# Kernel optimization log

Measured on AMD Instinct MI355X. Metric: run time of the kernel, lower is better.

The kernel has to match this reference:

```python
import jax, jax.numpy as jnp
import numpy as np

NEG = -1e9


def setup_inputs() -> dict:
    key = jax.random.key(0)
    ks = jax.random.split(key, 9)
    B, L, S, E = 8, 2048, 2048, 1024
    H, G, KD, VD = 16, 64, 1024, 1024
    return {
        "query": jax.random.normal(ks[0], (B, L, E), jnp.float32),
        "key": jax.random.normal(ks[1], (B, S, E), jnp.float32),
        "value": jax.random.normal(ks[2], (B, S, E), jnp.float32),
        "other": jnp.zeros((1,), jnp.float32),
        "key_padding_mask": jax.random.bernoulli(ks[3], 0.1, (B, S)),
        "nhead": H,
        "query_proj": jax.random.normal(ks[4], (1, E, KD), jnp.float32) * 0.02,
        "key_proj": jax.random.normal(ks[5], (1, E, KD), jnp.float32) * 0.02,
        "value_proj": jax.random.normal(ks[6], (1, E, VD), jnp.float32) * 0.02,
        "importance_proj": jax.random.normal(ks[7], (1, E, H * G), jnp.float32) * 0.02,
        "output_proj": jax.random.normal(ks[8], (1, VD, E), jnp.float32) * 0.02,
    }


def reference(query, key, value, other, key_padding_mask, nhead,
              query_proj, key_proj, value_proj, importance_proj, output_proj):
    B, L, E = query.shape
    S = key.shape[1]
    H = nhead
    KD = query_proj.shape[-1]
    VD = value_proj.shape[-1]
    Ek, Ev = KD // H, VD // H
    G = importance_proj.shape[-1] // H
    scale = 1.0 / jnp.sqrt(jnp.asarray(Ek, query.dtype))

    # projections -> (B, H, L/S, d)
    qs = (query @ query_proj[0]).reshape(B, L, H, Ek).transpose(0, 2, 1, 3)
    kk = (key @ key_proj[0]).reshape(B, S, H, Ek).transpose(0, 2, 1, 3)
    vs = (value @ value_proj[0]).reshape(B, S, H, Ev).transpose(0, 2, 1, 3)

    # importance-weighted global queries: softmax over L
    ips = (query @ importance_proj[0]).reshape(B, L, H, G).transpose(0, 2, 3, 1)  # (B,H,G,L)
    ips = jax.nn.softmax(ips, axis=-1)
    gqs = jnp.einsum('bhgl,bhld->bhgd', ips, qs)  # (B,H,G,Ek)

    # stage 1: global queries attend over all keys (shared attn for keys & values)
    g_scores = jnp.einsum('bhgd,bhsd->bhgs', gqs, kk) * scale  # (B,H,G,S)
    g_scores = jnp.where(key_padding_mask[:, None, None, :], NEG, g_scores)
    g_attn = jax.nn.softmax(g_scores, axis=-1)
    global_keys = jnp.einsum('bhgs,bhsd->bhgd', g_attn, kk)   # (B,H,G,Ek)
    global_values = jnp.einsum('bhgs,bhsd->bhgd', g_attn, vs)  # (B,H,G,Ev)

    # stage 2: local queries attend over G global keys/values
    l_scores = jnp.einsum('bhld,bhgd->bhlg', qs, global_keys) * scale  # (B,H,L,G)
    l_attn = jax.nn.softmax(l_scores, axis=-1)
    out = jnp.einsum('bhlg,bhgd->bhld', l_attn, global_values)  # (B,H,L,Ev)

    out = out.transpose(0, 2, 1, 3).reshape(B, L, H * Ev)
    out = out @ output_proj[0]  # (B,L,E)
    return (out, l_attn)
```

## Files before the change

kernel.cpp:

```cpp
#include <hip/hip_runtime.h>


typedef float f32x4 __attribute__((ext_vector_type(4)));
typedef _Float16 f16x8 __attribute__((ext_vector_type(8)));
typedef unsigned short u16;

#define DEV static __device__ __forceinline__

DEV u16 f2h(float x){
  _Float16 h = (_Float16)x;
  return __builtin_bit_cast(u16, h);
}
DEV float h2f(u16 u){
  return (float)__builtin_bit_cast(_Float16, u);
}
DEV void split1h(float x, u16 &h, u16 &l){
  h = f2h(x);
  l = f2h(x - h2f(h));
}
DEV unsigned pk2h(float a, float b){
  return (unsigned)f2h(a) | ((unsigned)f2h(b) << 16);
}

DEV void gload16(const u16* src, u16* dst_lds){
  __builtin_amdgcn_global_load_lds(
      (__attribute__((address_space(1))) void*)src,
      (__attribute__((address_space(3))) void*)dst_lds, 16, 0, 0);
}

__global__ __launch_bounds__(256)
void mask_norm(const unsigned char* __restrict__ src, unsigned char* __restrict__ dst, int n)
{
  const unsigned* w = (const unsigned*)src;
  const int tid = threadIdx.x;
  int local = 0;
  for (int i = tid; i < n/4; i += 256){
    unsigned v = w[i];
    if (v == 0x3F800000u) local |= 2;
    else if (v > 1u)      local |= 1;
  }
  __shared__ int red[256];
  red[tid] = local;
  __syncthreads();
  for (int s = 128; s; s >>= 1){
    if (tid < s) red[tid] |= red[tid+s];
    __syncthreads();
  }
  const int r = red[0];
  const int mode = (r & 2) ? 2 : ((r & 1) ? 1 : 0);
  for (int i = tid; i < n; i += 256){
    unsigned char v;
    if (mode == 1) v = src[i] ? 1 : 0;
    else           v = w[i]   ? 1 : 0;
    dst[i] = v;
  }
}

__global__ __launch_bounds__(256)
void conv_hi2(const float* __restrict__ x0, u16* __restrict__ h0,
              const float* __restrict__ x1, u16* __restrict__ h1, int n8)
{
  const float* x = blockIdx.z ? x1 : x0;
  u16* hi = blockIdx.z ? h1 : h0;
  const int i = blockIdx.x*256 + threadIdx.x;
  if (i >= n8) return;
  f32x4 a = ((const f32x4*)x)[2*i], b = ((const f32x4*)x)[2*i+1];
  uint4 uh;
  uh.x = pk2h(a[0], a[1]); uh.y = pk2h(a[2], a[3]);
  uh.z = pk2h(b[0], b[1]); uh.w = pk2h(b[2], b[3]);
  ((uint4*)hi)[i] = uh;
}

__global__ __launch_bounds__(256)
void conv_hi(const float* __restrict__ x, u16* __restrict__ hi, int n8)
{
  const int i = blockIdx.x*256 + threadIdx.x;
  if (i >= n8) return;
  f32x4 a = ((const f32x4*)x)[2*i], b = ((const f32x4*)x)[2*i+1];
  uint4 uh;
  uh.x = pk2h(a[0], a[1]); uh.y = pk2h(a[2], a[3]);
  uh.z = pk2h(b[0], b[1]); uh.w = pk2h(b[2], b[3]);
  ((uint4*)hi)[i] = uh;
}

__global__ __launch_bounds__(256)
void transpose_hi5(const float* __restrict__ s0, const float* __restrict__ s1,
                   const float* __restrict__ s2, const float* __restrict__ s3,
                   const float* __restrict__ s4,
                   u16* __restrict__ d0, u16* __restrict__ d1, u16* __restrict__ d2,
                   u16* __restrict__ d3, u16* __restrict__ d4)
{
  const int z = blockIdx.z;
  const float* Wsrc = z == 0 ? s0 : z == 1 ? s1 : z == 2 ? s2 : z == 3 ? s3 : s4;
  u16* Whi = z == 0 ? d0 : z == 1 ? d1 : z == 2 ? d2 : z == 3 ? d3 : d4;
  __shared__ float t[64][65];
  const int tid = threadIdx.x;
  const int n0 = blockIdx.x * 64, k0 = blockIdx.y * 64;
  #pragma unroll
  for (int it = 0; it < 16; ++it){
    int e = it*256 + tid, r = e >> 6, c = e & 63;
    t[r][c] = Wsrc[(long)(k0+r)*1024 + (n0+c)];
  }
  __syncthreads();
  #pragma unroll
  for (int it = 0; it < 16; ++it){
    int e = it*256 + tid, r = e >> 6, c = e & 63;
    Whi[(long)(n0+r)*1024 + (k0+c)] = f2h(t[c][r]);
  }
}

template<int TM, int TERMS, int CM, int EPI, int SWZ>
__global__ __launch_bounds__(256)
void gemm_g(const u16* __restrict__ Ah_g, const u16* __restrict__ Al_g,
            const u16* __restrict__ Bh_g,
            void* __restrict__ Cp, void* __restrict__ Cp2,
            const unsigned char* __restrict__ maskp,
            int K, int lda, int ldb, int ldc,
            long aB, long aH, long bB, long bH, long cB, long cH,
            int H2, int Ssz, float scale)
{
  constexpr int BN = 128, BK = 32;
  constexpr int WM = TM/2, WN = BN/2;
  constexpr int FM = WM/16, FN = WN/16;
  __shared__ __align__(16) u16 AhS[2][TM*BK];
  __shared__ __align__(16) u16 AlS[2][TERMS == 2 ? TM*BK : 8];
  __shared__ __align__(16) u16 BhS[2][BN*BK];

  const int tid = threadIdx.x;
  int bx = blockIdx.x, by = blockIdx.y;
  if constexpr (SWZ){
    const int gx = gridDim.x;
    const int nwg = gx * gridDim.y;
    const int q = nwg >> 3;
    const int flat = bx + gx * by;
    const int nf = (flat & 7) * q + (flat >> 3);
    bx = nf % gx; by = nf / gx;
  }
  const int batch = blockIdx.z;
  const int b = batch / H2, h = batch - b*H2;
  const long aOff = (long)b*aB + (long)h*aH;
  const long bOff = (long)b*bB + (long)h*bH;
  const long cOff = (long)b*cB + (long)h*cH;
  const int nBase = bx * BN;
  const int mBase = by * TM;
  const int wave = tid >> 6, lane = tid & 63;
  const int wm = wave >> 1, wn = wave & 1;
  const int cg8 = (lane & 3) * 8;
  const int rsub = lane >> 2;

  auto stage = [&](int buf, int k0){
    #pragma unroll
    for (int c = 0; c < TM/64; ++c){
      const int chunk = wave*(TM/64) + c;
      const long g = aOff + (long)(mBase + chunk*16 + rsub)*lda + k0 + cg8;
      gload16(Ah_g + g, &AhS[buf][chunk*512]);
      if constexpr (TERMS == 2) gload16(Al_g + g, &AlS[buf][chunk*512]);
    }
    #pragma unroll
    for (int c = 0; c < 2; ++c){
      const int chunk = wave*2 + c;
      const long g = bOff + (long)(nBase + chunk*16 + rsub)*ldb + k0 + cg8;
      gload16(Bh_g + g, &BhS[buf][chunk*512]);
    }
  };

  f32x4 acc[FM][FN] = {};

  stage(0, 0);
  __syncthreads();
  const int nk = K >> 5;
  for (int t = 0; t < nk; ++t){
    const int buf = t & 1;
    if (t + 1 < nk) stage(buf ^ 1, (t + 1) << 5);

    f16x8 ah[FM], al[FM], bh[FN];
    #pragma unroll
    for (int mi = 0; mi < FM; ++mi){
      const int off = (wm*WM + mi*16 + (lane & 15))*BK + (lane >> 4)*8;
      ah[mi] = *(const f16x8*)&AhS[buf][off];
      if constexpr (TERMS == 2) al[mi] = *(const f16x8*)&AlS[buf][off];
    }
    #pragma unroll
    for (int ni = 0; ni < FN; ++ni){
      const int off = (wn*WN + ni*16 + (lane & 15))*BK + (lane >> 4)*8;
      bh[ni] = *(const f16x8*)&BhS[buf][off];
    }
    #pragma unroll
    for (int mi = 0; mi < FM; ++mi)
      #pragma unroll
      for (int ni = 0; ni < FN; ++ni){
        acc[mi][ni] = __builtin_amdgcn_mfma_f32_16x16x32_f16(ah[mi], bh[ni], acc[mi][ni], 0, 0, 0);
        if constexpr (TERMS == 2)
          acc[mi][ni] = __builtin_amdgcn_mfma_f32_16x16x32_f16(al[mi], bh[ni], acc[mi][ni], 0, 0, 0);
      }
    __syncthreads();
  }

  const int cr = (lane >> 4) * 4, cc = lane & 15;
  #pragma unroll
  for (int mi = 0; mi < FM; ++mi)
    #pragma unroll
    for (int ni = 0; ni < FN; ++ni)
      #pragma unroll
      for (int r = 0; r < 4; ++r){
        const int row = mBase + wm*WM + mi*16 + cr + r;
        const int col = nBase + wn*WN + ni*16 + cc;
        float v = acc[mi][ni][r];
        if constexpr (EPI == 1){
          v *= scale;
          if (maskp[(long)b*Ssz + col]) v = -50000.0f;
        }
        const long ci = cOff + (long)row*ldc + col;
        if constexpr (CM == 0){
          ((float*)Cp)[ci] = v;
        } else {
          u16 hh, ll;
          split1h(v, hh, ll);
          ((u16*)Cp)[ci]  = hh;
          ((u16*)Cp2)[ci] = ll;
        }
      }
}

template<int NB>
__global__ __launch_bounds__(256)
void flash_agg(const u16* __restrict__ Sh_g, const u16* __restrict__ Sl_g,
               const u16* __restrict__ B1h_g, const u16* __restrict__ B1l_g,
               const u16* __restrict__ B2h_g, const u16* __restrict__ B2l_g,
               float* __restrict__ P1, float* __restrict__ P2,
               float* __restrict__ msm, float* __restrict__ mss,
               int K, int KC, int lda, int ldb,
               long aB, long aH, long bB, long bH, int H2, int nbatch)
{
  __shared__ __align__(16) u16 Ph[64][72], Pl[64][72];
  __shared__ __align__(16) u16 B1hS[64][72], B1lS[64][72];
  __shared__ __align__(16) u16 B2hS[NB==2?64:1][72], B2lS[NB==2?64:1][72];
  __shared__ float mS[64], sS[64], fS[64];
  const int tid = threadIdx.x;
  const int kc = blockIdx.x, batch = blockIdx.y;
  const int b = batch / H2, h = batch - b*H2;
  const long aOff = (long)b*aB + (long)h*aH;
  const long bOff = (long)b*bB + (long)h*bH;
  const int kchunk = K / KC, kbeg = kc * kchunk;
  const int wm = tid >> 6, lane = tid & 63;
  const int srow = tid >> 2, sq = tid & 3;

  if (tid < 64){ mS[tid] = -1e30f; sS[tid] = 0.f; }

  f32x4 acc1[4] = {}, acc2[4] = {};

  for (int ks = kbeg; ks < kbeg + kchunk; ks += 64){
    __syncthreads();
    #pragma unroll
    for (int it = 0; it < 4; ++it){
      const int e = it*256 + tid;
      const int lr = e >> 4, d0 = (e & 15) * 4;
      const long gm = bOff + (long)(ks + lr)*ldb + d0;
      ushort4 h4 = *(const ushort4*)(B1h_g + gm);
      ushort4 l4 = *(const ushort4*)(B1l_g + gm);
      B1hS[d0+0][lr]=h4.x; B1hS[d0+1][lr]=h4.y; B1hS[d0+2][lr]=h4.z; B1hS[d0+3][lr]=h4.w;
      B1lS[d0+0][lr]=l4.x; B1lS[d0+1][lr]=l4.y; B1lS[d0+2][lr]=l4.z; B1lS[d0+3][lr]=l4.w;
      if constexpr (NB == 2){
        ushort4 h42 = *(const ushort4*)(B2h_g + gm);
        ushort4 l42 = *(const ushort4*)(B2l_g + gm);
        B2hS[d0+0][lr]=h42.x; B2hS[d0+1][lr]=h42.y; B2hS[d0+2][lr]=h42.z; B2hS[d0+3][lr]=h42.w;
        B2lS[d0+0][lr]=l42.x; B2lS[d0+1][lr]=l42.y; B2lS[d0+2][lr]=l42.z; B2lS[d0+3][lr]=l42.w;
      }
    }

    float v[16];
    {
      const long ga = aOff + (long)srow*lda + ks + sq*16;
      uint4 ha = *(const uint4*)(Sh_g + ga);
      uint4 hb = *(const uint4*)(Sh_g + ga + 8);
      uint4 la = *(const uint4*)(Sl_g + ga);
      uint4 lb = *(const uint4*)(Sl_g + ga + 8);
      v[0]=h2f((u16)ha.x)+h2f((u16)la.x);  v[1]=h2f((u16)(ha.x>>16))+h2f((u16)(la.x>>16));
      v[2]=h2f((u16)ha.y)+h2f((u16)la.y);  v[3]=h2f((u16)(ha.y>>16))+h2f((u16)(la.y>>16));
      v[4]=h2f((u16)ha.z)+h2f((u16)la.z);  v[5]=h2f((u16)(ha.z>>16))+h2f((u16)(la.z>>16));
      v[6]=h2f((u16)ha.w)+h2f((u16)la.w);  v[7]=h2f((u16)(ha.w>>16))+h2f((u16)(la.w>>16));
      v[8]=h2f((u16)hb.x)+h2f((u16)lb.x);  v[9]=h2f((u16)(hb.x>>16))+h2f((u16)(lb.x>>16));
      v[10]=h2f((u16)hb.y)+h2f((u16)lb.y); v[11]=h2f((u16)(hb.y>>16))+h2f((u16)(lb.y>>16));
      v[12]=h2f((u16)hb.z)+h2f((u16)lb.z); v[13]=h2f((u16)(hb.z>>16))+h2f((u16)(lb.z>>16));
      v[14]=h2f((u16)hb.w)+h2f((u16)lb.w); v[15]=h2f((u16)(hb.w>>16))+h2f((u16)(lb.w>>16));
    }
    float mx = v[0];
    #pragma unroll
    for (int i = 1; i < 16; ++i) mx = fmaxf(mx, v[i]);
    mx = fmaxf(mx, __shfl_xor(mx, 1));
    mx = fmaxf(mx, __shfl_xor(mx, 2));
    const float mold = mS[srow];
    const float mnew = fmaxf(mold, mx);
    float sum = 0.f;
    u16 ph[16], pl[16];
    #pragma unroll
    for (int i = 0; i < 16; ++i){
      float e = __expf(v[i] - mnew);
      sum += e;
      split1h(e, ph[i], pl[i]);
    }
    sum += __shfl_xor(sum, 1);
    sum += __shfl_xor(sum, 2);
    if (sq == 0){
      const float f = __expf(mold - mnew);
      sS[srow] = sS[srow] * f + sum;
      mS[srow] = mnew;
      fS[srow] = f;
    }
    {
      uint4 uh0, uh1, ul0, ul1;
      uh0.x=(unsigned)ph[0]|((unsigned)ph[1]<<16);  uh0.y=(unsigned)ph[2]|((unsigned)ph[3]<<16);
      uh0.z=(unsigned)ph[4]|((unsigned)ph[5]<<16);  uh0.w=(unsigned)ph[6]|((unsigned)ph[7]<<16);
      uh1.x=(unsigned)ph[8]|((unsigned)ph[9]<<16);  uh1.y=(unsigned)ph[10]|((unsigned)ph[11]<<16);
      uh1.z=(unsigned)ph[12]|((unsigned)ph[13]<<16);uh1.w=(unsigned)ph[14]|((unsigned)ph[15]<<16);
      ul0.x=(unsigned)pl[0]|((unsigned)pl[1]<<16);  ul0.y=(unsigned)pl[2]|((unsigned)pl[3]<<16);
      ul0.z=(unsigned)pl[4]|((unsigned)pl[5]<<16);  ul0.w=(unsigned)pl[6]|((unsigned)pl[7]<<16);
      ul1.x=(unsigned)pl[8]|((unsigned)pl[9]<<16);  ul1.y=(unsigned)pl[10]|((unsigned)pl[11]<<16);
      ul1.z=(unsigned)pl[12]|((unsigned)pl[13]<<16);ul1.w=(unsigned)pl[14]|((unsigned)pl[15]<<16);
      *(uint4*)&Ph[srow][sq*16]     = uh0;
      *(uint4*)&Ph[srow][sq*16 + 8] = uh1;
      *(uint4*)&Pl[srow][sq*16]     = ul0;
      *(uint4*)&Pl[srow][sq*16 + 8] = ul1;
    }
    __syncthreads();

    float fr4[4];
    #pragma unroll
    for (int r = 0; r < 4; ++r) fr4[r] = fS[wm*16 + (lane >> 4)*4 + r];
    #pragma unroll
    for (int ni = 0; ni < 4; ++ni)
      #pragma unroll
      for (int r = 0; r < 4; ++r){
        acc1[ni][r] *= fr4[r];
        if constexpr (NB == 2) acc2[ni][r] *= fr4[r];
      }
    #pragma unroll
    for (int k0 = 0; k0 < 64; k0 += 32){
      const int ko = k0 + (lane >> 4)*8;
      const int fr = lane & 15;
      f16x8 a_h = *(const f16x8*)&Ph[wm*16 + fr][ko];
      f16x8 a_l = *(const f16x8*)&Pl[wm*16 + fr][ko];
      #pragma unroll
      for (int ni = 0; ni < 4; ++ni){
        f16x8 b_h = *(const f16x8*)&B1hS[ni*16 + fr][ko];
        f16x8 b_l = *(const f16x8*)&B1lS[ni*16 + fr][ko];
        acc1[ni] = __builtin_amdgcn_mfma_f32_16x16x32_f16(a_h, b_h, acc1[ni], 0, 0, 0);
        acc1[ni] = __builtin_amdgcn_mfma_f32_16x16x32_f16(a_l, b_h, acc1[ni], 0, 0, 0);
        acc1[ni] = __builtin_amdgcn_mfma_f32_16x16x32_f16(a_h, b_l, acc1[ni], 0, 0, 0);
        if constexpr (NB == 2){
          f16x8 c_h = *(const f16x8*)&B2hS[ni*16 + fr][ko];
          f16x8 c_l = *(const f16x8*)&B2lS[ni*16 + fr][ko];
          acc2[ni] = __builtin_amdgcn_mfma_f32_16x16x32_f16(a_h, c_h, acc2[ni], 0, 0, 0);
          acc2[ni] = __builtin_amdgcn_mfma_f32_16x16x32_f16(a_l, c_h, acc2[ni], 0, 0, 0);
          acc2[ni] = __builtin_amdgcn_mfma_f32_16x16x32_f16(a_h, c_l, acc2[ni], 0, 0, 0);
        }
      }
    }
  }

  const long po = ((long)(kc*nbatch + batch) << 12);
  const int cr = (lane >> 4) * 4, cc = lane & 15;
  #pragma unroll
  for (int ni = 0; ni < 4; ++ni)
    #pragma unroll
    for (int r = 0; r < 4; ++r){
      const int g = wm*16 + cr + r, d = ni*16 + cc;
      P1[po + g*64 + d] = acc1[ni][r];
      if constexpr (NB == 2) P2[po + g*64 + d] = acc2[ni][r];
    }
  if (tid < 64){
    msm[((long)kc*nbatch + batch)*64 + tid] = mS[tid];
    mss[((long)kc*nbatch + batch)*64 + tid] = sS[tid];
  }
}

template<int NB, int KC>
__global__ __launch_bounds__(256)
void flash_combine(const float* __restrict__ P1, const float* __restrict__ P2,
                   const float* __restrict__ msm, const float* __restrict__ mss,
                   u16* __restrict__ o1h, u16* __restrict__ o1l,
                   u16* __restrict__ o2h, u16* __restrict__ o2l, int nbatch)
{
  const int batch = blockIdx.x;
  const int tid = threadIdx.x;
  const int g = tid >> 2, dq = (tid & 3) * 16;
  float m[KC], s[KC], w[KC];
  float M = -1e30f;
  #pragma unroll
  for (int c = 0; c < KC; ++c){
    m[c] = msm[((long)c*nbatch + batch)*64 + g];
    s[c] = mss[((long)c*nbatch + batch)*64 + g];
    M = fmaxf(M, m[c]);
  }
  float den = 0.f;
  #pragma unroll
  for (int c = 0; c < KC; ++c){ w[c] = __expf(m[c] - M); den += s[c]*w[c]; }
  const float inv = 1.0f / den;
  #pragma unroll
  for (int c = 0; c < KC; ++c) w[c] *= inv;
  const long oo = (long)batch*4096 + g*64 + dq;
  #pragma unroll
  for (int nb = 0; nb < NB; ++nb){
    const float* Pa = nb ? P2 : P1;
    u16* oh = nb ? o2h : o1h;
    u16* ol = nb ? o2l : o1l;
    u16 hh[16], ll[16];
    #pragma unroll
    for (int j = 0; j < 4; ++j){
      f32x4 a = {0.f, 0.f, 0.f, 0.f};
      #pragma unroll
      for (int c = 0; c < KC; ++c){
        f32x4 p = *(const f32x4*)(Pa + (((long)c*nbatch + batch) << 12) + g*64 + dq + j*4);
        a += p * w[c];
      }
      #pragma unroll
      for (int e = 0; e < 4; ++e) split1h(a[e], hh[j*4+e], ll[j*4+e]);
    }
    uint4 uh0, uh1, ul0, ul1;
    uh0.x=(unsigned)hh[0]|((unsigned)hh[1]<<16);  uh0.y=(unsigned)hh[2]|((unsigned)hh[3]<<16);
    uh0.z=(unsigned)hh[4]|((unsigned)hh[5]<<16);  uh0.w=(unsigned)hh[6]|((unsigned)hh[7]<<16);
    uh1.x=(unsigned)hh[8]|((unsigned)hh[9]<<16);  uh1.y=(unsigned)hh[10]|((unsigned)hh[11]<<16);
    uh1.z=(unsigned)hh[12]|((unsigned)hh[13]<<16);uh1.w=(unsigned)hh[14]|((unsigned)hh[15]<<16);
    ul0.x=(unsigned)ll[0]|((unsigned)ll[1]<<16);  ul0.y=(unsigned)ll[2]|((unsigned)ll[3]<<16);
    ul0.z=(unsigned)ll[4]|((unsigned)ll[5]<<16);  ul0.w=(unsigned)ll[6]|((unsigned)ll[7]<<16);
    ul1.x=(unsigned)ll[8]|((unsigned)ll[9]<<16);  ul1.y=(unsigned)ll[10]|((unsigned)ll[11]<<16);
    ul1.z=(unsigned)ll[12]|((unsigned)ll[13]<<16);ul1.w=(unsigned)ll[14]|((unsigned)ll[15]<<16);
    *(uint4*)(oh + oo)     = uh0;
    *(uint4*)(oh + oo + 8) = uh1;
    *(uint4*)(ol + oo)     = ul0;
    *(uint4*)(ol + oo + 8) = ul1;
  }
}

__global__ __launch_bounds__(256)
void stage2_mfma(const u16* __restrict__ qhi, const u16* __restrict__ qlo,
                 const u16* __restrict__ gkh_g, const u16* __restrict__ gkl_g,
                 const u16* __restrict__ gvh_g, const u16* __restrict__ gvl_g,
                 float* __restrict__ lattn, u16* __restrict__ ahi,
                 float scale)
{
  __shared__ __align__(16) u16 Ah[128][72];
  __shared__ __align__(16) u16 Al[128][72];
  __shared__ __align__(16) u16 Bh[64][72];
  __shared__ __align__(16) u16 Bl[64][72];
  const int tid = threadIdx.x;
  const int bh = blockIdx.y;
  const int b = bh >> 4, h = bh & 15;
  const int l0 = blockIdx.x * 128;
  const int wm = tid >> 6, lane = tid & 63;

  const long qbase = ((long)b*2048 + l0)*1024 + h*64;
  #pragma unroll
  for (int it = 0; it < 4; ++it){
    const int e = it*256 + tid, row = e >> 3, s = e & 7;
    const long g = qbase + (long)row*1024 + s*8;
    *(uint4*)&Ah[row][s*8] = *(const uint4*)(qhi + g);
    *(uint4*)&Al[row][s*8] = *(const uint4*)(qlo + g);
  }
  const long gb = (long)bh * 4096;
  #pragma unroll
  for (int it = 0; it < 2; ++it){
    const int e = it*256 + tid, gr = e >> 3, s = e & 7;
    *(uint4*)&Bh[gr][s*8] = *(const uint4*)(gkh_g + gb + gr*64 + s*8);
    *(uint4*)&Bl[gr][s*8] = *(const uint4*)(gkl_g + gb + gr*64 + s*8);
  }
  __syncthreads();

  f32x4 acc[2][4] = {};
  #pragma unroll
  for (int k0 = 0; k0 < 64; k0 += 32){
    f16x8 a_h[2], a_l[2], b_h[4], b_l[4];
    #pragma unroll
    for (int mi = 0; mi < 2; ++mi){
      const int row = wm*32 + mi*16 + (lane & 15);
      a_h[mi] = *(const f16x8*)&Ah[row][k0 + (lane >> 4)*8];
      a_l[mi] = *(const f16x8*)&Al[row][k0 + (lane >> 4)*8];
    }
    #pragma unroll
    for (int ni = 0; ni < 4; ++ni){
      const int nr = ni*16 + (lane & 15);
      b_h[ni] = *(const f16x8*)&Bh[nr][k0 + (lane >> 4)*8];
      b_l[ni] = *(const f16x8*)&Bl[nr][k0 + (lane >> 4)*8];
    }
    #pragma unroll
    for (int mi = 0; mi < 2; ++mi)
      #pragma unroll
      for (int ni = 0; ni < 4; ++ni){
        acc[mi][ni] = __builtin_amdgcn_mfma_f32_16x16x32_f16(a_h[mi], b_h[ni], acc[mi][ni], 0, 0, 0);
        acc[mi][ni] = __builtin_amdgcn_mfma_f32_16x16x32_f16(a_l[mi], b_h[ni], acc[mi][ni], 0, 0, 0);
        acc[mi][ni] = __builtin_amdgcn_mfma_f32_16x16x32_f16(a_h[mi], b_l[ni], acc[mi][ni], 0, 0, 0);
      }
  }
  __syncthreads();

  #pragma unroll
  for (int it = 0; it < 4; ++it){
    const int e = it*256 + tid;
    const int gr = e >> 4, d0 = (e & 15) * 4;
    ushort4 vh = *(const ushort4*)(gvh_g + gb + gr*64 + d0);
    ushort4 vl = *(const ushort4*)(gvl_g + gb + gr*64 + d0);
    Bh[d0+0][gr] = vh.x; Bh[d0+1][gr] = vh.y; Bh[d0+2][gr] = vh.z; Bh[d0+3][gr] = vh.w;
    Bl[d0+0][gr] = vl.x; Bl[d0+1][gr] = vl.y; Bl[d0+2][gr] = vl.z; Bl[d0+3][gr] = vl.w;
  }

  #pragma unroll
  for (int mi = 0; mi < 2; ++mi){
    #pragma unroll
    for (int r = 0; r < 4; ++r){
      float v0 = acc[mi][0][r]*scale, v1 = acc[mi][1][r]*scale;
      float v2 = acc[mi][2][r]*scale, v3 = acc[mi][3][r]*scale;
      float mx = fmaxf(fmaxf(v0,v1), fmaxf(v2,v3));
      #pragma unroll
      for (int off = 1; off < 16; off <<= 1) mx = fmaxf(mx, __shfl_xor(mx, off, 16));
      float e0 = __expf(v0-mx), e1 = __expf(v1-mx), e2 = __expf(v2-mx), e3 = __expf(v3-mx);
      float sum = (e0+e1) + (e2+e3);
      #pragma unroll
      for (int off = 1; off < 16; off <<= 1) sum += __shfl_xor(sum, off, 16);
      const float inv = 1.0f / sum;
      e0 *= inv; e1 *= inv; e2 *= inv; e3 *= inv;
      const int lrow = wm*32 + mi*16 + (lane >> 4)*4 + r;
      float* lp = lattn + ((long)bh*2048 + l0 + lrow)*64 + (lane & 15);
      lp[0] = e0; lp[16] = e1; lp[32] = e2; lp[48] = e3;
      u16 hh, ll;
      split1h(e0, hh, ll); Ah[lrow][ 0 + (lane&15)] = hh; Al[lrow][ 0 + (lane&15)] = ll;
      split1h(e1, hh, ll); Ah[lrow][16 + (lane&15)] = hh; Al[lrow][16 + (lane&15)] = ll;
      split1h(e2, hh, ll); Ah[lrow][32 + (lane&15)] = hh; Al[lrow][32 + (lane&15)] = ll;
      split1h(e3, hh, ll); Ah[lrow][48 + (lane&15)] = hh; Al[lrow][48 + (lane&15)] = ll;
    }
  }
  __syncthreads();

  f32x4 o[2][4] = {};
  #pragma unroll
  for (int k0 = 0; k0 < 64; k0 += 32){
    f16x8 p_h[2], p_l[2], b_h[4], b_l[4];
    #pragma unroll
    for (int mi = 0; mi < 2; ++mi){
      const int row = wm*32 + mi*16 + (lane & 15);
      p_h[mi] = *(const f16x8*)&Ah[row][k0 + (lane >> 4)*8];
      p_l[mi] = *(const f16x8*)&Al[row][k0 + (lane >> 4)*8];
    }
    #pragma unroll
    for (int ni = 0; ni < 4; ++ni){
      const int nr = ni*16 + (lane & 15);
      b_h[ni] = *(const f16x8*)&Bh[nr][k0 + (lane >> 4)*8];
      b_l[ni] = *(const f16x8*)&Bl[nr][k0 + (lane >> 4)*8];
    }
    #pragma unroll
    for (int mi = 0; mi < 2; ++mi)
      #pragma unroll
      for (int ni = 0; ni < 4; ++ni){
        o[mi][ni] = __builtin_amdgcn_mfma_f32_16x16x32_f16(p_h[mi], b_h[ni], o[mi][ni], 0, 0, 0);
        o[mi][ni] = __builtin_amdgcn_mfma_f32_16x16x32_f16(p_l[mi], b_h[ni], o[mi][ni], 0, 0, 0);
        o[mi][ni] = __builtin_amdgcn_mfma_f32_16x16x32_f16(p_h[mi], b_l[ni], o[mi][ni], 0, 0, 0);
      }
  }

  #pragma unroll
  for (int mi = 0; mi < 2; ++mi)
    #pragma unroll
    for (int ni = 0; ni < 4; ++ni)
      #pragma unroll
      for (int r = 0; r < 4; ++r){
        const int lrow = wm*32 + mi*16 + (lane >> 4)*4 + r;
        const int d = ni*16 + (lane & 15);
        const long oidx = ((long)b*2048 + l0 + lrow)*1024 + h*64 + d;
        ahi[oidx] = f2h(o[mi][ni][r]);
      }
}

extern "C" void kernel_launch(void* const* d_in, const int* in_sizes, int n_in,
                              void* d_out, int out_size, void* d_ws, size_t ws_size,
                              hipStream_t stream)
{
  const float* query = (const float*)d_in[0];
  const float* key   = (const float*)d_in[1];
  const float* value = (const float*)d_in[2];
  const unsigned char* mask_raw = (const unsigned char*)d_in[4];
  const float* Wq = (const float*)d_in[6];
  const float* Wk = (const float*)d_in[7];
  const float* Wv = (const float*)d_in[8];
  const float* Wi = (const float*)d_in[9];
  const float* Wo = (const float*)d_in[10];
  float* out0 = (float*)d_out;
  float* out1 = out0 + 16777216;

  char* ws = (char*)d_ws;
  u16* WoT_hi = (u16*)(ws + 0);
  float* msm_q = (float*)(ws + (2L<<20));
  float* mss_q = (float*)(ws + (2L<<20) + 262144);
  float* msm_g = (float*)(ws + (3L<<20));
  float* mss_g = (float*)(ws + (3L<<20) + 262144);
  u16* WqT_hi = (u16*)(ws + (4L<<20));
  unsigned char* mask_ws = (unsigned char*)(ws + (6L<<20));
  float* part1 = (float*)(ws + (4L<<20));
  u16* WkT_hi = (u16*)(ws + (8L<<20));
  u16* WvT_hi = (u16*)(ws + (12L<<20));
  float* part2 = (float*)(ws + (12L<<20));
  u16* gqs_hi = (u16*)(ws + (16L<<20));
  u16* gqs_lo = (u16*)(ws + (17L<<20));
  u16* WiT_hi = (u16*)(ws + (18L<<20));
  u16* qp_hi  = (u16*)(ws + (20L<<20));
  u16* vp_hi  = qp_hi;
  u16* gsc_hi = (u16*)(ws + (20L<<20));
  u16* kp_hi  = (u16*)(ws + (52L<<20));
  u16* gsc_lo = (u16*)(ws + (52L<<20));
  u16* qs_hi  = (u16*)(ws + (84L<<20));
  u16* qs_lo  = (u16*)(ws + (116L<<20));
  float* partg = (float*)(ws + (148L<<20));
  u16* vs_hi  = (u16*)(ws + (148L<<20));
  u16* vs_lo  = (u16*)(ws + (180L<<20));
  u16* ips_hi = (u16*)(ws + (212L<<20));
  u16* ips_lo = (u16*)(ws + (244L<<20));
  u16* kk_hi  = (u16*)(ws + (212L<<20));
  u16* kk_lo  = (u16*)(ws + (244L<<20));
  u16* gk_hi  = (u16*)(ws + (212L<<20));
  u16* gk_lo  = (u16*)(ws + (213L<<20));
  u16* gv_hi  = (u16*)(ws + (214L<<20));
  u16* gv_lo  = (u16*)(ws + (215L<<20));
  u16* attn_hi = (u16*)(ws + (244L<<20));

  const dim3 blk(256);
  const float scale = 0.125f;

  mask_norm<<<1, blk, 0, stream>>>(mask_raw, mask_ws, 16384);

  transpose_hi5<<<dim3(16,16,5), blk, 0, stream>>>(Wq, Wk, Wv, Wi, Wo,
      WqT_hi, WkT_hi, WvT_hi, WiT_hi, WoT_hi);

  conv_hi2<<<dim3(8192,1,2), blk, 0, stream>>>(query, qp_hi, key, kp_hi, 2097152);

  gemm_g<128,1,1,0,1><<<dim3(8,128,1), blk, 0, stream>>>(
      qp_hi, nullptr, WqT_hi, qs_hi, qs_lo, nullptr,
      1024, 1024,1024,1024, 0,0, 0,0, 0,0, 1, 2048, 1.f);

  gemm_g<128,1,1,0,0><<<dim3(16,8,8), blk, 0, stream>>>(
      WiT_hi, nullptr, qp_hi, ips_hi, ips_lo, nullptr,
      1024, 1024,1024,2048, 0,0, 2097152L,0, 2097152L,0, 1, 2048, 1.f);

  flash_agg<1><<<dim3(4,128), blk, 0, stream>>>(
      ips_hi, ips_lo, qs_hi, qs_lo, nullptr, nullptr,
      partg, nullptr, msm_q, mss_q,
      2048, 4, 2048, 1024, 2097152L, 131072L, 2097152L, 64L, 16, 128);
  flash_combine<1,4><<<128, blk, 0, stream>>>(
      partg, nullptr, msm_q, mss_q, gqs_hi, gqs_lo, nullptr, nullptr, 128);

  gemm_g<128,1,1,0,1><<<dim3(8,128,1), blk, 0, stream>>>(
      kp_hi, nullptr, WkT_hi, kk_hi, kk_lo, nullptr,
      1024, 1024,1024,1024, 0,0, 0,0, 0,0, 1, 2048, 1.f);

  conv_hi<<<8192, blk, 0, stream>>>(value, vp_hi, 2097152);
  gemm_g<128,1,1,0,1><<<dim3(8,128,1), blk, 0, stream>>>(
      vp_hi, nullptr, WvT_hi, vs_hi, vs_lo, nullptr,
      1024, 1024,1024,1024, 0,0, 0,0, 0,0, 1, 2048, 1.f);

  gemm_g<64,2,1,1,0><<<dim3(16,1,128), blk, 0, stream>>>(
      gqs_hi, gqs_lo, kk_hi, gsc_hi, gsc_lo, mask_ws,
      64, 64,1024,2048, 65536L,4096L, 2097152L,64L, 2097152L,131072L, 16, 2048, scale);

  flash_agg<2><<<dim3(4,128), blk, 0, stream>>>(
      gsc_hi, gsc_lo, kk_hi, kk_lo, vs_hi, vs_lo,
      part1, part2, msm_g, mss_g,
      2048, 4, 2048, 1024, 2097152L, 131072L, 2097152L, 64L, 16, 128);
  flash_combine<2,4><<<128, blk, 0, stream>>>(
      part1, part2, msm_g, mss_g, gk_hi, gk_lo, gv_hi, gv_lo, 128);

  stage2_mfma<<<dim3(16,128), blk, 0, stream>>>(qs_hi, qs_lo, gk_hi, gk_lo,
      gv_hi, gv_lo, out1, attn_hi, scale);

  gemm_g<128,1,0,0,1><<<dim3(8,128,1), blk, 0, stream>>>(
      attn_hi, nullptr, WoT_hi, out0, nullptr, nullptr,
      1024, 1024,1024,1024, 0,0, 0,0, 0,0, 1, 2048, 1.f);

  (void)in_sizes; (void)n_in; (void)out_size; (void)ws_size;
}
```

Baseline: 539.7 us.

## Merge paired projection GEMMs into single launches and fuse fp32-to-fp16 conversion for K/V

Adds a gemm_pair kernel that runs two independent GEMMs in one grid: the Q projection together with the importance projection, and the K projection together with the V projection. For K and V the kernel reads the fp32 inputs directly and converts them to fp16 in registers before the LDS store, which removes the separate conversion passes and their extra global traffic. It also remaps block indices to spread work across XCD groups. The trade-off is register-staged A loads with a software double buffer, which may raise register pressure and expose load latency.

```diff
diff --git a/kernel.cpp b/kernel.cpp
--- a/kernel.cpp
+++ b/kernel.cpp
@@ -54,21 +54,6 @@
     else           v = w[i]   ? 1 : 0;
     dst[i] = v;
   }
-}
-
-__global__ __launch_bounds__(256)
-void conv_hi2(const float* __restrict__ x0, u16* __restrict__ h0,
-              const float* __restrict__ x1, u16* __restrict__ h1, int n8)
-{
-  const float* x = blockIdx.z ? x1 : x0;
-  u16* hi = blockIdx.z ? h1 : h0;
-  const int i = blockIdx.x*256 + threadIdx.x;
-  if (i >= n8) return;
-  f32x4 a = ((const f32x4*)x)[2*i], b = ((const f32x4*)x)[2*i+1];
-  uint4 uh;
-  uh.x = pk2h(a[0], a[1]); uh.y = pk2h(a[2], a[3]);
-  uh.z = pk2h(b[0], b[1]); uh.w = pk2h(b[2], b[3]);
-  ((uint4*)hi)[i] = uh;
 }
 
 __global__ __launch_bounds__(256)
@@ -222,6 +207,145 @@
       }
 }
 
+struct PArg {
+  const void* Ap;
+  const u16*  Bh;
+  u16* Ch; u16* Cl;
+  long bB, cB;
+  int lda, ldb, ldc;
+  int nbx, nby;
+};
+
+template<int TM, int AMODE>
+__global__ __launch_bounds__(256)
+void gemm_pair(PArg a0, PArg a1, int n0, int K)
+{
+  constexpr int BN = 128, BK = 32;
+  constexpr int WM = TM/2, WN = BN/2;
+  constexpr int FM = WM/16, FN = WN/16;
+  constexpr int NC = TM/64;
+  __shared__ __align__(16) u16 AhS[2][TM*BK];
+  __shared__ __align__(16) u16 BhS[2][BN*BK];
+
+  const int tid = threadIdx.x;
+  const int gid = blockIdx.x;
+  const PArg P = (gid < n0) ? a0 : a1;
+  int lid = (gid < n0) ? gid : gid - n0;
+  const int gsz = (gid < n0) ? n0 : ((int)gridDim.x - n0);
+  {
+    const int q = gsz >> 3;
+    lid = (lid & 7) * q + (lid >> 3);
+  }
+  const int bx = lid % P.nbx;
+  const int rest = lid / P.nbx;
+  const int by = rest % P.nby;
+  const int z  = rest / P.nby;
+  const long bOff = (long)z * P.bB;
+  const long cOff = (long)z * P.cB;
+  const int nBase = bx * BN;
+  const int mBase = by * TM;
+  const int wave = tid >> 6, lane = tid & 63;
+  const int wm = wave >> 1, wn = wave & 1;
+  const int cg8 = (lane & 3) * 8;
+  const int rsub = lane >> 2;
+
+  const u16* Au = (const u16*)P.Ap;
+  const float* Af = (const float*)P.Ap;
+
+  auto stageB = [&](int buf, int k0){
+    #pragma unroll
+    for (int c = 0; c < 2; ++c){
+      const int chunk = wave*2 + c;
+      const long g = bOff + (long)(nBase + chunk*16 + rsub)*P.ldb + k0 + cg8;
+      gload16(P.Bh + g, &BhS[buf][chunk*512]);
+    }
+  };
+  auto stageA_g = [&](int buf, int k0){
+    #pragma unroll
+    for (int c = 0; c < NC; ++c){
+      const int chunk = wave*NC + c;
+      const long g = (long)(mBase + chunk*16 + rsub)*P.lda + k0 + cg8;
+      gload16(Au + g, &AhS[buf][chunk*512]);
+    }
+  };
+
+  f32x4 acc[FM][FN] = {};
+  f32x4 sA0[NC], sA1[NC];
+
+  auto loadA_f = [&](int k0){
+    #pragma unroll
+    for (int c = 0; c < NC; ++c){
+      const int chunk = wave*NC + c;
+      const long g = (long)(mBase + chunk*16 + rsub)*P.lda + k0 + cg8;
+      sA0[c] = *(const f32x4*)(Af + g);
+      sA1[c] = *(const f32x4*)(Af + g + 4);
+    }
+  };
+  auto writeA_f = [&](int buf){
+    #pragma unroll
+    for (int c = 0; c < NC; ++c){
+      const int chunk = wave*NC + c;
+      uint4 u;
+      u.x = pk2h(sA0[c][0], sA0[c][1]); u.y = pk2h(sA0[c][2], sA0[c][3]);
+      u.z = pk2h(sA1[c][0], sA1[c][1]); u.w = pk2h(sA1[c][2], sA1[c][3]);
+      *(uint4*)&AhS[buf][chunk*512 + (long)lane*8] = u;
+    }
+  };
+
+  stageB(0, 0);
+  if constexpr (AMODE == 1) stageA_g(0, 0);
+  else { loadA_f(0); writeA_f(0); }
+  __syncthreads();
+
+  const int nk = K >> 5;
+  for (int t = 0; t < nk; ++t){
+    const int buf = t & 1;
+    if (t + 1 < nk){
+      stageB(buf ^ 1, (t + 1) << 5);
+      if constexpr (AMODE == 1) stageA_g(buf ^ 1, (t + 1) << 5);
+      else loadA_f((t + 1) << 5);
+    }
+
+    f16x8 ah[FM], bh[FN];
+    #pragma unroll
+    for (int mi = 0; mi < FM; ++mi){
+      const int off = (wm*WM + mi*16 + (lane & 15))*BK + (lane >> 4)*8;
+      ah[mi] = *(const f16x8*)&AhS[buf][off];
+    }
+    #pragma unroll
+    for (int ni = 0; ni < FN; ++ni){
+      const int off = (wn*WN + ni*16 + (lane & 15))*BK + (lane >> 4)*8;
+      bh[ni] = *(const f16x8*)&BhS[buf][off];
+    }
+    #pragma unroll
+    for (int mi = 0; mi < FM; ++mi)
+      #pragma unroll
+      for (int ni = 0; ni < FN; ++ni)
+        acc[mi][ni] = __builtin_amdgcn_mfma_f32_16x16x32_f16(ah[mi], bh[ni], acc[mi][ni], 0, 0, 0);
+
+    if constexpr (AMODE == 0){
+      if (t + 1 < nk) writeA_f(buf ^ 1);
+    }
+    __syncthreads();
+  }
+
+  const int cr = (lane >> 4) * 4, cc = lane & 15;
+  #pragma unroll
+  for (int mi = 0; mi < FM; ++mi)
+    #pragma unroll
+    for (int ni = 0; ni < FN; ++ni)
+      #pragma unroll
+      for (int r = 0; r < 4; ++r){
+        const int row = mBase + wm*WM + mi*16 + cr + r;
+        const int col = nBase + wn*WN + ni*16 + cc;
+        const long ci = cOff + (long)row*P.ldc + col;
+        u16 hh, ll;
+        split1h(acc[mi][ni][r], hh, ll);
+        P.Ch[ci] = hh;
+        P.Cl[ci] = ll;
+      }
+}
+
 template<int NB>
 __global__ __launch_bounds__(256)
 void flash_agg(const u16* __restrict__ Sh_g, const u16* __restrict__ Sl_g,
@@ -601,9 +725,7 @@
   u16* gqs_lo = (u16*)(ws + (17L<<20));
   u16* WiT_hi = (u16*)(ws + (18L<<20));
   u16* qp_hi  = (u16*)(ws + (20L<<20));
-  u16* vp_hi  = qp_hi;
   u16* gsc_hi = (u16*)(ws + (20L<<20));
-  u16* kp_hi  = (u16*)(ws + (52L<<20));
   u16* gsc_lo = (u16*)(ws + (52L<<20));
   u16* qs_hi  = (u16*)(ws + (84L<<20));
   u16* qs_lo  = (u16*)(ws + (116L<<20));
@@ -624,19 +746,17 @@
   const float scale = 0.125f;
 
   mask_norm<<<1, blk, 0, stream>>>(mask_raw, mask_ws, 16384);
-
   transpose_hi5<<<dim3(16,16,5), blk, 0, stream>>>(Wq, Wk, Wv, Wi, Wo,
       WqT_hi, WkT_hi, WvT_hi, WiT_hi, WoT_hi);
-
-  conv_hi2<<<dim3(8192,1,2), blk, 0, stream>>>(query, qp_hi, key, kp_hi, 2097152);
-
-  gemm_g<128,1,1,0,1><<<dim3(8,128,1), blk, 0, stream>>>(
-      qp_hi, nullptr, WqT_hi, qs_hi, qs_lo, nullptr,
-      1024, 1024,1024,1024, 0,0, 0,0, 0,0, 1, 2048, 1.f);
-
-  gemm_g<128,1,1,0,0><<<dim3(16,8,8), blk, 0, stream>>>(
-      WiT_hi, nullptr, qp_hi, ips_hi, ips_lo, nullptr,
-      1024, 1024,1024,2048, 0,0, 2097152L,0, 2097152L,0, 1, 2048, 1.f);
+  conv_hi<<<8192, blk, 0, stream>>>(query, qp_hi, 2097152);
+
+  {
+    PArg g0 = { qp_hi,  WqT_hi, qs_hi,  qs_lo,  0L, 0L,
+                1024, 1024, 1024, 8, 128 };
+    PArg g1 = { WiT_hi, qp_hi,  ips_hi, ips_lo, 2097152L, 2097152L,
+                1024, 1024, 2048, 16, 8 };
+    gemm_pair<128,1><<<2048, blk, 0, stream>>>(g0, g1, 1024, 1024);
+  }
 
   flash_agg<1><<<dim3(4,128), blk, 0, stream>>>(
       ips_hi, ips_lo, qs_hi, qs_lo, nullptr, nullptr,
@@ -645,14 +765,11 @@
   flash_combine<1,4><<<128, blk, 0, stream>>>(
       partg, nullptr, msm_q, mss_q, gqs_hi, gqs_lo, nullptr, nullptr, 128);
 
-  gemm_g<128,1,1,0,1><<<dim3(8,128,1), blk, 0, stream>>>(
-      kp_hi, nullptr, WkT_hi, kk_hi, kk_lo, nullptr,
-      1024, 1024,1024,1024, 0,0, 0,0, 0,0, 1, 2048, 1.f);
-
-  conv_hi<<<8192, blk, 0, stream>>>(value, vp_hi, 2097152);
-  gemm_g<128,1,1,0,1><<<dim3(8,128,1), blk, 0, stream>>>(
-      vp_hi, nullptr, WvT_hi, vs_hi, vs_lo, nullptr,
-      1024, 1024,1024,1024, 0,0, 0,0, 0,0, 1, 2048, 1.f);
+  {
+    PArg g0 = { key,   WkT_hi, kk_hi, kk_lo, 0L, 0L, 1024, 1024, 1024, 8, 128 };
+    PArg g1 = { value, WvT_hi, vs_hi, vs_lo, 0L, 0L, 1024, 1024, 1024, 8, 128 };
+    gemm_pair<128,0><<<2048, blk, 0, stream>>>(g0, g1, 1024, 1024);
+  }
 
   gemm_g<64,2,1,1,0><<<dim3(16,1,128), blk, 0, stream>>>(
       gqs_hi, gqs_lo, kk_hi, gsc_hi, gsc_lo, mask_ws,
```

After: 517.0 us, median of 2. 4.2% less time.
